# Performance work log

Measured on AMD Instinct MI355X. Metric: run time of the kernel, lower is better.

## Reference

```python
import jax, jax.numpy as jnp
from jax import lax
import numpy as np

T, B, I, H = 512, 64, 512, 512


def setup_inputs() -> dict:
    key = jax.random.key(0)
    k0, k1, k2, k3, k4 = jax.random.split(key, 5)
    s = 1.0 / np.sqrt(H)  # PyTorch LSTM init range
    x = jax.random.normal(k0, (T, B, I), dtype=jnp.float32)
    W_ih = jax.random.uniform(k1, (4 * H, I), jnp.float32, -s, s)
    W_hh = jax.random.uniform(k2, (4 * H, H), jnp.float32, -s, s)
    b_ih = jax.random.uniform(k3, (4 * H,), jnp.float32, -s, s)
    b_hh = jax.random.uniform(k4, (4 * H,), jnp.float32, -s, s)
    return {"x": x, "W_ih": W_ih, "W_hh": W_hh, "b_ih": b_ih, "b_hh": b_hh}


def reference(x, W_ih, W_hh, b_ih, b_hh):
    # x: [T, B, I] (seq-first, like nn.LSTM with batch_first=False)
    Bv = x.shape[1]
    Hv = W_hh.shape[1]
    # Precompute input projections for all timesteps: [T, B, 4H]
    x_proj = jnp.einsum('tbi,gi->tbg', x, W_ih) + b_ih + b_hh

    def step(carry, xp):
        h, c = carry
        gates = xp + h @ W_hh.T  # [B, 4H]
        i, f, g, o = jnp.split(gates, 4, axis=-1)  # PyTorch gate order i,f,g,o
        i = jax.nn.sigmoid(i)
        f = jax.nn.sigmoid(f)
        g = jnp.tanh(g)
        o = jax.nn.sigmoid(o)
        c = f * c + i * g
        h = o * jnp.tanh(c)
        return (h, c), h

    h0 = jnp.zeros((Bv, Hv), dtype=x.dtype)
    c0 = jnp.zeros((Bv, Hv), dtype=x.dtype)
    _, ys = lax.scan(step, (h0, c0), x_proj)
    return ys  # [T, B, H]
```

## Files before the change

### kernel.cpp

```cpp
#include <hip/hip_runtime.h>


#define T_STEPS 512
#define BATCH   64
#define HID     512
#define NB      64

typedef short bf16x8 __attribute__((ext_vector_type(8)));
typedef float f32x4  __attribute__((ext_vector_type(4)));

struct U16B { unsigned long long x, y; };

__device__ __forceinline__ unsigned short f2bf(float f) {
    unsigned int u = __builtin_bit_cast(unsigned int, f);
    u += 0x7FFFu + ((u >> 16) & 1u);
    return (unsigned short)(u >> 16);
}
__device__ __forceinline__ unsigned int pack2(float lo, float hi) {
    return (unsigned int)f2bf(lo) | ((unsigned int)f2bf(hi) << 16);
}
__device__ __forceinline__ uint4 cvt8(const float* __restrict__ p) {
    float4 f0 = *(const float4*)p;
    float4 f1 = *(const float4*)(p + 4);
    uint4 r;
    r.x = pack2(f0.x, f0.y);
    r.y = pack2(f0.z, f0.w);
    r.z = pack2(f1.x, f1.y);
    r.w = pack2(f1.z, f1.w);
    return r;
}
__device__ __forceinline__ bf16x8 load_h16(const unsigned short* p) {
    const unsigned long long* q = (const unsigned long long*)p;
    U16B v;
    v.x = __hip_atomic_load(q,     __ATOMIC_RELAXED, __HIP_MEMORY_SCOPE_AGENT);
    v.y = __hip_atomic_load(q + 1, __ATOMIC_RELAXED, __HIP_MEMORY_SCOPE_AGENT);
    return __builtin_bit_cast(bf16x8, v);
}
__device__ __forceinline__ float sigmoidf_(float x) {
    return 1.0f / (1.0f + __expf(-x));
}
__device__ __forceinline__ float tanhf_(float x) {
    x = fminf(fmaxf(x, -15.f), 15.f);
    float e = __expf(2.0f * x);
    return (e - 1.0f) / (e + 1.0f);
}

extern "C" __global__ void __launch_bounds__(256, 1)
lstm_fused(const float* __restrict__ x,
           const float* __restrict__ W_ih,
           const float* __restrict__ W_hh,
           const float* __restrict__ b_ih,
           const float* __restrict__ b_hh,
           float* __restrict__ out,
           unsigned int* __restrict__ flags,
           unsigned short* __restrict__ hbuf)
{
    __shared__ uint4 sB[2][2][16][64];

    const int blk  = blockIdx.x;
    const int tid  = threadIdx.x;
    const int w    = tid >> 6;
    const int lane = tid & 63;
    const int l15  = lane & 15;
    const int quad = lane >> 4;
    const int hc0  = blk * 8;

    for (int u = tid; u < 2 * 16 * 64; u += 256) {
        int nt   = u >> 10;
        int kk   = (u >> 6) & 15;
        int ln   = u & 63;
        int c    = (ln & 15) + (nt << 4);
        int grow = ((c >> 3) << 9) + hc0 + (c & 7);
        int k0   = kk * 32 + ((ln >> 4) << 3);
        sB[0][nt][kk][ln] = cvt8(W_ih + grow * 512 + k0);
        sB[1][nt][kk][ln] = cvt8(W_hh + grow * 512 + k0);
    }

    float bias0, bias1;
    {
        int c0 = l15,      g0 = ((c0 >> 3) << 9) + hc0 + (c0 & 7);
        int c1 = l15 + 16, g1 = ((c1 >> 3) << 9) + hc0 + (c1 & 7);
        bias0 = b_ih[g0] + b_hh[g0];
        bias1 = b_ih[g1] + b_hh[g1];
    }
    __syncthreads();

    float cst[4] = {0.f, 0.f, 0.f, 0.f};
    const int aoff = (((w << 4) + l15) * 512) + (quad << 3);
    long long budget = 200000000LL;

    for (int t = 0; t < T_STEPS; ++t) {
        f32x4 acc0 = {0.f, 0.f, 0.f, 0.f};
        f32x4 acc1 = {0.f, 0.f, 0.f, 0.f};

        const float* xt = x + (size_t)t * (BATCH * 512) + aoff;
#pragma unroll
        for (int kk = 0; kk < 16; ++kk) {
            bf16x8 a  = __builtin_bit_cast(bf16x8, cvt8(xt + kk * 32));
            bf16x8 b0 = __builtin_bit_cast(bf16x8, sB[0][0][kk][lane]);
            bf16x8 b1 = __builtin_bit_cast(bf16x8, sB[0][1][kk][lane]);
            acc0 = __builtin_amdgcn_mfma_f32_16x16x32_bf16(a, b0, acc0, 0, 0, 0);
            acc1 = __builtin_amdgcn_mfma_f32_16x16x32_bf16(a, b1, acc1, 0, 0, 0);
        }

        if (t > 0) {
            if (w == 0) {
                const unsigned int* fp = flags + (size_t)(t - 1) * NB + lane;
                while (budget > 0) {
                    unsigned int v = __hip_atomic_load(fp, __ATOMIC_RELAXED,
                                                       __HIP_MEMORY_SCOPE_AGENT);
                    if (__all(v != 0)) break;
                    --budget;
                }
            }
            __syncthreads();

            const unsigned short* hp = hbuf + (size_t)((t - 1) & 1) * (BATCH * HID) + aoff;
#pragma unroll
            for (int kk = 0; kk < 16; ++kk) {
                bf16x8 a  = load_h16(hp + kk * 32);
                bf16x8 b0 = __builtin_bit_cast(bf16x8, sB[1][0][kk][lane]);
                bf16x8 b1 = __builtin_bit_cast(bf16x8, sB[1][1][kk][lane]);
                acc0 = __builtin_amdgcn_mfma_f32_16x16x32_bf16(a, b0, acc0, 0, 0, 0);
                acc1 = __builtin_amdgcn_mfma_f32_16x16x32_bf16(a, b1, acc1, 0, 0, 0);
            }
        }

        float gi[4], gf[4], gg[4], go[4];
#pragma unroll
        for (int r = 0; r < 4; ++r) {
            float a0 = acc0[r] + bias0;
            float a1 = acc1[r] + bias1;
            float p0 = __shfl_xor(a0, 8, 64);
            float p1 = __shfl_xor(a1, 8, 64);
            gi[r] = a0; gg[r] = a1; gf[r] = p0; go[r] = p1;
        }
        if (l15 < 8) {
            const int rbase = (w << 4) + (quad << 2);
            float*          op = out  + (size_t)t * (BATCH * HID) + hc0 + l15;
            unsigned short* hb = hbuf + (size_t)(t & 1) * (BATCH * HID) + hc0 + l15;
#pragma unroll
            for (int r = 0; r < 4; ++r) {
                float iv = sigmoidf_(gi[r]);
                float fv = sigmoidf_(gf[r]);
                float gv = tanhf_(gg[r]);
                float ov = sigmoidf_(go[r]);
                cst[r] = fv * cst[r] + iv * gv;
                float hv = ov * tanhf_(cst[r]);
                op[(size_t)(rbase + r) * HID] = hv;
                __hip_atomic_store(hb + (size_t)(rbase + r) * HID, f2bf(hv),
                                   __ATOMIC_RELAXED, __HIP_MEMORY_SCOPE_AGENT);
            }
        }

        __syncthreads();
        if (tid == 0) {
            __hip_atomic_store(flags + (size_t)t * NB + blk, 1u,
                               __ATOMIC_RELAXED, __HIP_MEMORY_SCOPE_AGENT);
        }
    }
}

extern "C" void kernel_launch(void* const* d_in, const int* in_sizes, int n_in,
                              void* d_out, int out_size, void* d_ws, size_t ws_size,
                              hipStream_t stream) {
    const float* x    = (const float*)d_in[0];
    const float* W_ih = (const float*)d_in[1];
    const float* W_hh = (const float*)d_in[2];
    const float* b_ih = (const float*)d_in[3];
    const float* b_hh = (const float*)d_in[4];
    float* out = (float*)d_out;

    unsigned int*   flags = (unsigned int*)d_ws;
    const size_t    flag_bytes = (size_t)T_STEPS * NB * sizeof(unsigned int);
    unsigned short* hbuf  = (unsigned short*)((char*)d_ws + flag_bytes);

    hipMemsetAsync(flags, 0, flag_bytes, stream);

    hipLaunchKernelGGL(lstm_fused, dim3(NB), dim3(256), 0, stream,
                       x, W_ih, W_hh, b_ih, b_hh, out, flags, hbuf);
}
```

Baseline: 4.893 ms.

## Stage h in LDS and write it in a k-chunked packed layout with 16B stores

Each wave now collects its bf16 hidden outputs in shared memory and writes them to the global exchange buffer as 16-byte atomic stores, replacing scattered 2-byte atomic stores. The buffer is laid out in k-chunk-major order so that each block's slice is contiguous. Reads of h are remapped to match the new layout. The fp32 output stores now come after the flag release, which takes them off the critical path of the inter-block dependency. The spin budget is also lowered, and an explicit vmcnt wait before the barrier makes sure the stores are done before the flag is set.

```diff
diff --git a/kernel.cpp b/kernel.cpp
--- a/kernel.cpp
+++ b/kernel.cpp
@@ -29,12 +29,18 @@
     r.w = pack2(f1.z, f1.w);
     return r;
 }
-__device__ __forceinline__ bf16x8 load_h16(const unsigned short* p) {
+__device__ __forceinline__ bf16x8 load_h16(const void* p) {
     const unsigned long long* q = (const unsigned long long*)p;
     U16B v;
     v.x = __hip_atomic_load(q,     __ATOMIC_RELAXED, __HIP_MEMORY_SCOPE_AGENT);
     v.y = __hip_atomic_load(q + 1, __ATOMIC_RELAXED, __HIP_MEMORY_SCOPE_AGENT);
     return __builtin_bit_cast(bf16x8, v);
+}
+__device__ __forceinline__ void store_cg16(void* p, uint4 v) {
+    unsigned long long* q = (unsigned long long*)p;
+    U16B u = __builtin_bit_cast(U16B, v);
+    __hip_atomic_store(q,     u.x, __ATOMIC_RELAXED, __HIP_MEMORY_SCOPE_AGENT);
+    __hip_atomic_store(q + 1, u.y, __ATOMIC_RELAXED, __HIP_MEMORY_SCOPE_AGENT);
 }
 __device__ __forceinline__ float sigmoidf_(float x) {
     return 1.0f / (1.0f + __expf(-x));
@@ -56,6 +62,7 @@
            unsigned short* __restrict__ hbuf)
 {
     __shared__ uint4 sB[2][2][16][64];
+    __shared__ __align__(16) unsigned short sH[4][16][8];
 
     const int blk  = blockIdx.x;
     const int tid  = threadIdx.x;
@@ -87,7 +94,9 @@
 
     float cst[4] = {0.f, 0.f, 0.f, 0.f};
     const int aoff = (((w << 4) + l15) * 512) + (quad << 3);
-    long long budget = 200000000LL;
+    char* const hb_base = (char*)hbuf;
+    const int   hread_off = (quad << 10) + (((w << 4) + l15) << 4);
+    long long budget = 50000000LL;
 
     for (int t = 0; t < T_STEPS; ++t) {
         f32x4 acc0 = {0.f, 0.f, 0.f, 0.f};
@@ -115,10 +124,10 @@
             }
             __syncthreads();
 
-            const unsigned short* hp = hbuf + (size_t)((t - 1) & 1) * (BATCH * HID) + aoff;
+            const char* hp = hb_base + (((t - 1) & 1) << 16) + hread_off;
 #pragma unroll
             for (int kk = 0; kk < 16; ++kk) {
-                bf16x8 a  = load_h16(hp + kk * 32);
+                bf16x8 a  = load_h16(hp + (kk << 12));
                 bf16x8 b0 = __builtin_bit_cast(bf16x8, sB[1][0][kk][lane]);
                 bf16x8 b1 = __builtin_bit_cast(bf16x8, sB[1][1][kk][lane]);
                 acc0 = __builtin_amdgcn_mfma_f32_16x16x32_bf16(a, b0, acc0, 0, 0, 0);
@@ -135,10 +144,8 @@
             float p1 = __shfl_xor(a1, 8, 64);
             gi[r] = a0; gg[r] = a1; gf[r] = p0; go[r] = p1;
         }
+        float hv[4];
         if (l15 < 8) {
-            const int rbase = (w << 4) + (quad << 2);
-            float*          op = out  + (size_t)t * (BATCH * HID) + hc0 + l15;
-            unsigned short* hb = hbuf + (size_t)(t & 1) * (BATCH * HID) + hc0 + l15;
 #pragma unroll
             for (int r = 0; r < 4; ++r) {
                 float iv = sigmoidf_(gi[r]);
@@ -146,17 +153,30 @@
                 float gv = tanhf_(gg[r]);
                 float ov = sigmoidf_(go[r]);
                 cst[r] = fv * cst[r] + iv * gv;
-                float hv = ov * tanhf_(cst[r]);
-                op[(size_t)(rbase + r) * HID] = hv;
-                __hip_atomic_store(hb + (size_t)(rbase + r) * HID, f2bf(hv),
-                                   __ATOMIC_RELAXED, __HIP_MEMORY_SCOPE_AGENT);
+                hv[r] = ov * tanhf_(cst[r]);
+                sH[w][(quad << 2) + r][l15] = f2bf(hv[r]);
             }
         }
-
+        asm volatile("s_waitcnt lgkmcnt(0)" ::: "memory");
+        if (lane < 16) {
+            uint4 v = *(const uint4*)&sH[w][lane][0];
+            char* dst = hb_base + ((t & 1) << 16) + (blk << 10)
+                        + (((w << 4) + lane) << 4);
+            store_cg16(dst, v);
+        }
+        asm volatile("s_waitcnt vmcnt(0)" ::: "memory");
         __syncthreads();
         if (tid == 0) {
             __hip_atomic_store(flags + (size_t)t * NB + blk, 1u,
                                __ATOMIC_RELAXED, __HIP_MEMORY_SCOPE_AGENT);
+        }
+
+        if (l15 < 8) {
+            const int rbase = (w << 4) + (quad << 2);
+            float* op = out + (size_t)t * (BATCH * HID) + hc0 + l15;
+#pragma unroll
+            for (int r = 0; r < 4; ++r)
+                op[(size_t)(rbase + r) * HID] = hv[r];
         }
     }
 }
@@ -175,7 +195,7 @@
     const size_t    flag_bytes = (size_t)T_STEPS * NB * sizeof(unsigned int);
     unsigned short* hbuf  = (unsigned short*)((char*)d_ws + flag_bytes);
 
-    hipMemsetAsync(flags, 0, flag_bytes, stream);
+    (void)hipMemsetAsync(flags, 0, flag_bytes, stream);
 
     hipLaunchKernelGGL(lstm_fused, dim3(NB), dim3(256), 0, stream,
                        x, W_ih, W_hh, b_ih, b_hh, out, flags, hbuf);
```

Result: faster. 4.321 ms (-11.7%).
